# Optimization experiments

Measured on AMD Instinct MI355X. Metric: run time of the kernel, lower is better.

The kernel has to match this reference:

```python
import jax, jax.numpy as jnp
import numpy as np

DIM = 768
HEADS = 12
HIDDEN = 3072
EPS = 1e-5


def _layernorm(x, g, b):
    mu = jnp.mean(x, axis=-1, keepdims=True)
    var = jnp.var(x, axis=-1, keepdims=True)
    return (x - mu) * jax.lax.rsqrt(var + EPS) * g + b


def setup_inputs() -> dict:
    key = jax.random.key(0)
    ks = jax.random.split(key, 10)
    s_in = 1.0 / np.sqrt(DIM)
    s_hid = 1.0 / np.sqrt(HIDDEN)
    return {
        "x": jax.random.normal(ks[0], (8, 1024, DIM), dtype=jnp.float32),
        "ln1_g": jnp.ones((DIM,), jnp.float32),
        "ln1_b": jnp.zeros((DIM,), jnp.float32),
        "qkv_w": jax.random.uniform(ks[1], (DIM, 3 * DIM), jnp.float32, -s_in, s_in),
        "qkv_b": jnp.zeros((3 * DIM,), jnp.float32),
        "proj_w": jax.random.uniform(ks[2], (DIM, DIM), jnp.float32, -s_in, s_in),
        "proj_b": jnp.zeros((DIM,), jnp.float32),
        "ln2_g": jnp.ones((DIM,), jnp.float32),
        "ln2_b": jnp.zeros((DIM,), jnp.float32),
        "fc1_w": jax.random.uniform(ks[3], (DIM, HIDDEN), jnp.float32, -s_in, s_in),
        "fc1_b": jnp.zeros((HIDDEN,), jnp.float32),
        "fc2_w": jax.random.uniform(ks[4], (HIDDEN, DIM), jnp.float32, -s_hid, s_hid),
        "fc2_b": jnp.zeros((DIM,), jnp.float32),
    }


def reference(x, ln1_g, ln1_b, qkv_w, qkv_b, proj_w, proj_b,
              ln2_g, ln2_b, fc1_w, fc1_b, fc2_w, fc2_b):
    B, N, C = x.shape
    H = HEADS
    Dh = C // H
    scale = Dh ** -0.5

    # --- attention sublayer (pre-norm) ---
    h = _layernorm(x, ln1_g, ln1_b)
    qkv = h @ qkv_w + qkv_b  # [B,N,3C]
    qkv = qkv.reshape(B, N, 3, H, Dh)
    q = qkv[:, :, 0].transpose(0, 2, 1, 3)  # [B,H,N,Dh]
    k = qkv[:, :, 1].transpose(0, 2, 1, 3)
    v = qkv[:, :, 2].transpose(0, 2, 1, 3)
    attn = jax.nn.softmax(jnp.einsum('bhnd,bhmd->bhnm', q, k) * scale, axis=-1)
    o = jnp.einsum('bhnm,bhmd->bhnd', attn, v)  # [B,H,N,Dh]
    o = o.transpose(0, 2, 1, 3).reshape(B, N, C)
    x = x + (o @ proj_w + proj_b)

    # --- MLP sublayer (pre-norm) ---
    h = _layernorm(x, ln2_g, ln2_b)
    h = jax.nn.gelu(h @ fc1_w + fc1_b, approximate=False)
    x = x + (h @ fc2_w + fc2_b)
    return x
```

## Files before the change

kernel.cpp:

```cpp
#include <hip/hip_runtime.h>
#include <math.h>

#define DIM    768
#define HEADS  12
#define HIDDEN 3072
#define SEQ    1024
#define NTOK   8192
#define QKVLD  2304

typedef __bf16 bf16_t;
typedef __bf16 bf16x4 __attribute__((ext_vector_type(4)));
typedef __bf16 bf16x8 __attribute__((ext_vector_type(8)));
typedef float  f32x4  __attribute__((ext_vector_type(4)));

union ABFrag { bf16x4 h[2]; bf16x8 v; };

__device__ __forceinline__ void gload16(const void* g, void* l) {
  __builtin_amdgcn_global_load_lds(
      (const __attribute__((address_space(1))) void*)g,
      (__attribute__((address_space(3))) void*)l, 16, 0, 0);
}

__device__ __forceinline__ f32x4 mfma16(bf16x8 a, bf16x8 b, f32x4 c) {
  return __builtin_amdgcn_mfma_f32_16x16x32_bf16(a, b, c, 0, 0, 0);
}

__device__ __forceinline__ ABFrag load_frag(const bf16_t* rowp, int g) {
  ABFrag f;
  f.h[0] = *(const bf16x4*)(rowp + 4 * g);
  f.h[1] = *(const bf16x4*)(rowp + 4 * g + 16);
  return f;
}

__device__ __forceinline__ bf16x8 ldsfrag(const bf16_t* base, int row, int lc) {
  return *(const bf16x8*)(base + row * 64 + ((lc ^ (row & 7)) << 3));
}

__device__ __forceinline__ float gelu_f(float v) {
  float u = v * fmaf(v * v, 0.0356774081f, 0.7978845608f);
  u = fminf(u, 15.0f);
  float t = __builtin_amdgcn_exp2f(u * 2.8853900817779268f);
  return v * t * __builtin_amdgcn_rcpf(t + 1.0f);
}

__global__ __launch_bounds__(256) void ln_kernel(
    const float* __restrict__ x, const float* __restrict__ gw,
    const float* __restrict__ bw, bf16_t* __restrict__ out) {
  const int row = blockIdx.x * 4 + (threadIdx.x >> 6);
  const int lane = threadIdx.x & 63;
  const float* xr = x + (size_t)row * DIM;
  f32x4 v[3];
  float s = 0.f, s2 = 0.f;
  #pragma unroll
  for (int i = 0; i < 3; ++i) {
    v[i] = *(const f32x4*)(xr + lane * 4 + i * 256);
    #pragma unroll
    for (int j = 0; j < 4; ++j) { s += v[i][j]; s2 += v[i][j] * v[i][j]; }
  }
  #pragma unroll
  for (int o = 32; o > 0; o >>= 1) {
    s += __shfl_xor(s, o);
    s2 += __shfl_xor(s2, o);
  }
  const float mu  = s * (1.0f / DIM);
  const float var = s2 * (1.0f / DIM) - mu * mu;
  const float rs  = rsqrtf(var + 1e-5f);
  bf16_t* orow = out + (size_t)row * DIM;
  #pragma unroll
  for (int i = 0; i < 3; ++i) {
    const int c = lane * 4 + i * 256;
    f32x4 gv = *(const f32x4*)(gw + c);
    f32x4 bv = *(const f32x4*)(bw + c);
    bf16x4 o4;
    #pragma unroll
    for (int j = 0; j < 4; ++j)
      o4[j] = (bf16_t)((v[i][j] - mu) * rs * gv[j] + bv[j]);
    *(bf16x4*)(orow + c) = o4;
  }
}

__global__ __launch_bounds__(256) void wtrans_kernel(
    const float* __restrict__ W, bf16_t* __restrict__ Wt, int K, int N) {
  __shared__ float tile[32][33];
  const int tx = threadIdx.x, ty = threadIdx.y;
  const int n0 = blockIdx.x * 32, k0 = blockIdx.y * 32;
  #pragma unroll
  for (int i = 0; i < 4; ++i)
    tile[ty + i * 8][tx] = W[(size_t)(k0 + ty + i * 8) * N + n0 + tx];
  __syncthreads();
  #pragma unroll
  for (int i = 0; i < 4; ++i)
    Wt[(size_t)(n0 + ty + i * 8) * K + k0 + tx] = (bf16_t)tile[tx][ty + i * 8];
}

__global__ __launch_bounds__(256) void vtrans_kernel(
    const bf16_t* __restrict__ qkv, bf16_t* __restrict__ vt) {
  __shared__ bf16_t tile[64][65];
  const int bh = blockIdx.y, b = bh / HEADS, h = bh % HEADS;
  const int n0 = blockIdx.x * 64;
  const int t = threadIdx.x;
  const int c = t & 63, rr = t >> 6;
  const bf16_t* src = qkv + (size_t)(b * SEQ + n0) * QKVLD + 2 * DIM + h * 64;
  #pragma unroll
  for (int i = 0; i < 16; ++i)
    tile[c][rr + i * 4] = src[(size_t)(rr + i * 4) * QKVLD + c];
  __syncthreads();
  bf16_t* dst = vt + (size_t)bh * 64 * SEQ + n0;
  #pragma unroll
  for (int i = 0; i < 16; ++i)
    dst[(size_t)(rr + i * 4) * SEQ + c] = tile[rr + i * 4][c];
}

template <int MODE>
__global__ __launch_bounds__(256) void gemm_sb(
    const bf16_t* __restrict__ A, const bf16_t* __restrict__ Bt,
    int N, int K,
    const float* __restrict__ bias, const float* __restrict__ res,
    void* __restrict__ outv, int gx) {
  __shared__ bf16_t sA[128 * 64];
  __shared__ bf16_t sB[128 * 64];
  const int tid = threadIdx.x;
  const int lane = tid & 63;
  const int wid = tid >> 6;
  const int g = lane >> 4, r16 = lane & 15;

  const int nwg = gridDim.x;
  const int cpx = nwg >> 3;
  const int sw = (blockIdx.x & 7) * cpx + (blockIdx.x >> 3);
  const int bx = sw % gx, by = sw / gx;
  const int row0 = by * 128, col0 = bx * 128;
  const int wr = (wid >> 1) * 64, wc = (wid & 1) * 64;

  f32x4 acc[4][4];
  #pragma unroll
  for (int m = 0; m < 4; ++m)
    #pragma unroll
    for (int n = 0; n < 4; ++n) acc[m][n] = f32x4{0.f, 0.f, 0.f, 0.f};

  const int kSteps = K >> 6;
  for (int kt = 0; kt < kSteps; ++kt) {
    __syncthreads();
    #pragma unroll
    for (int rnd = 0; rnd < 4; ++rnd) {
      const int c = rnd * 256 + tid;
      const int row = c >> 3, scp = (c & 7) ^ (row & 7);
      gload16(A + (size_t)(row0 + row) * K + (size_t)kt * 64 + scp * 8, &sA[c * 8]);
    }
    #pragma unroll
    for (int rnd = 0; rnd < 4; ++rnd) {
      const int c = rnd * 256 + tid;
      const int row = c >> 3, scp = (c & 7) ^ (row & 7);
      gload16(Bt + (size_t)(col0 + row) * K + (size_t)kt * 64 + scp * 8, &sB[c * 8]);
    }
    __syncthreads();
    bf16x8 af[4][2], bfr[4][2];
    #pragma unroll
    for (int m = 0; m < 4; ++m)
      #pragma unroll
      for (int kk = 0; kk < 2; ++kk)
        af[m][kk] = ldsfrag(sA, wr + m * 16 + r16, kk * 4 + g);
    #pragma unroll
    for (int n = 0; n < 4; ++n)
      #pragma unroll
      for (int kk = 0; kk < 2; ++kk)
        bfr[n][kk] = ldsfrag(sB, wc + n * 16 + r16, kk * 4 + g);
    #pragma unroll
    for (int kk = 0; kk < 2; ++kk)
      #pragma unroll
      for (int m = 0; m < 4; ++m)
        #pragma unroll
        for (int n = 0; n < 4; ++n)
          acc[m][n] = mfma16(af[m][kk], bfr[n][kk], acc[m][n]);
  }

  #pragma unroll
  for (int m = 0; m < 4; ++m) {
    const int rowb = row0 + wr + m * 16 + 4 * g;
    #pragma unroll
    for (int n = 0; n < 4; ++n) {
      const int col = col0 + wc + n * 16 + r16;
      const float bv = bias[col];
      #pragma unroll
      for (int r = 0; r < 4; ++r) {
        const size_t idx = (size_t)(rowb + r) * N + col;
        float v = acc[m][n][r] + bv;
        if (MODE == 0) {
          ((bf16_t*)outv)[idx] = (bf16_t)v;
        } else if (MODE == 1) {
          ((float*)outv)[idx] = v + res[idx];
        } else {
          ((bf16_t*)outv)[idx] = (bf16_t)gelu_f(v);
        }
      }
    }
  }
}

template <int MODE>
__global__ __launch_bounds__(256) void gemm_db(
    const bf16_t* __restrict__ A, const bf16_t* __restrict__ Bt,
    int N, int K,
    const float* __restrict__ bias, const float* __restrict__ res,
    void* __restrict__ outv, int gx) {
  __shared__ bf16_t sA[2][128 * 64];
  __shared__ bf16_t sB[2][128 * 64];
  const int tid = threadIdx.x;
  const int lane = tid & 63;
  const int wid = tid >> 6;
  const int g = lane >> 4, r16 = lane & 15;

  const int nwg = gridDim.x;
  const int cpx = nwg >> 3;
  const int sw = (blockIdx.x & 7) * cpx + (blockIdx.x >> 3);
  const int bx = sw % gx, by = sw / gx;
  const int row0 = by * 128, col0 = bx * 128;
  const int wr = (wid >> 1) * 64, wc = (wid & 1) * 64;

  auto stage = [&](int p, int kt) {
    #pragma unroll
    for (int rnd = 0; rnd < 4; ++rnd) {
      const int c = rnd * 256 + tid;
      const int row = c >> 3, scp = (c & 7) ^ (row & 7);
      gload16(A + (size_t)(row0 + row) * K + (size_t)kt * 64 + scp * 8,
              &sA[p][c * 8]);
    }
    #pragma unroll
    for (int rnd = 0; rnd < 4; ++rnd) {
      const int c = rnd * 256 + tid;
      const int row = c >> 3, scp = (c & 7) ^ (row & 7);
      gload16(Bt + (size_t)(col0 + row) * K + (size_t)kt * 64 + scp * 8,
              &sB[p][c * 8]);
    }
  };

  f32x4 acc[4][4];
  #pragma unroll
  for (int m = 0; m < 4; ++m)
    #pragma unroll
    for (int n = 0; n < 4; ++n) acc[m][n] = f32x4{0.f, 0.f, 0.f, 0.f};

  const int kSteps = K >> 6;
  stage(0, 0);
  for (int kt = 0; kt < kSteps; ++kt) {
    const int cur = kt & 1;
    __syncthreads();
    if (kt + 1 < kSteps) stage(cur ^ 1, kt + 1);

    bf16x8 af[4][2], bfr[4][2];
    #pragma unroll
    for (int m = 0; m < 4; ++m)
      #pragma unroll
      for (int kk = 0; kk < 2; ++kk)
        af[m][kk] = ldsfrag(&sA[cur][0], wr + m * 16 + r16, kk * 4 + g);
    #pragma unroll
    for (int n = 0; n < 4; ++n)
      #pragma unroll
      for (int kk = 0; kk < 2; ++kk)
        bfr[n][kk] = ldsfrag(&sB[cur][0], wc + n * 16 + r16, kk * 4 + g);
    #pragma unroll
    for (int kk = 0; kk < 2; ++kk)
      #pragma unroll
      for (int m = 0; m < 4; ++m)
        #pragma unroll
        for (int n = 0; n < 4; ++n)
          acc[m][n] = mfma16(af[m][kk], bfr[n][kk], acc[m][n]);
  }

  #pragma unroll
  for (int m = 0; m < 4; ++m) {
    const int rowb = row0 + wr + m * 16 + 4 * g;
    #pragma unroll
    for (int n = 0; n < 4; ++n) {
      const int col = col0 + wc + n * 16 + r16;
      const float bv = bias[col];
      #pragma unroll
      for (int r = 0; r < 4; ++r) {
        const size_t idx = (size_t)(rowb + r) * N + col;
        float v = acc[m][n][r] + bv;
        if (MODE == 0) {
          ((bf16_t*)outv)[idx] = (bf16_t)v;
        } else if (MODE == 1) {
          ((float*)outv)[idx] = v + res[idx];
        } else {
          ((bf16_t*)outv)[idx] = (bf16_t)gelu_f(v);
        }
      }
    }
  }
}

__global__ __launch_bounds__(512) void attn_kernel(
    const bf16_t* __restrict__ qkv, const bf16_t* __restrict__ vt,
    bf16_t* __restrict__ o) {
  __shared__ bf16_t kbuf[2][64 * 64];
  __shared__ bf16_t vbuf[2][64 * 64];
  const int bh = blockIdx.x, b = bh / HEADS, h = bh % HEADS;
  const int q0 = blockIdx.y * 128;
  const int tid = threadIdx.x, lane = tid & 63, wid = tid >> 6;
  const int g = lane >> 4, r16 = lane & 15;

  const bf16_t* qptr = qkv + (size_t)b * SEQ * QKVLD + h * 64;
  const bf16_t* kptr = qptr + DIM;
  const bf16_t* vtp  = vt + (size_t)bh * 64 * SEQ;

  ABFrag aq[2];
  {
    const bf16_t* qr = qptr + (size_t)(q0 + wid * 16 + r16) * QKVLD;
    aq[0] = load_frag(qr, g);
    aq[1] = load_frag(qr + 32, g);
  }

  int off[4][2][2];
  #pragma unroll
  for (int i = 0; i < 4; ++i) {
    const int row = i * 16 + r16, s = row & 7, rp = row * 64;
    #pragma unroll
    for (int e2 = 0; e2 < 2; ++e2) {
      const int o0 = e2 * 32 + 4 * g, o1 = o0 + 16;
      off[i][e2][0] = rp + ((((o0 >> 3) ^ s) << 3) | (o0 & 7));
      off[i][e2][1] = rp + ((((o1 >> 3) ^ s) << 3) | (o1 & 7));
    }
  }

  float lacc = 0.f;
  f32x4 acco[4];
  #pragma unroll
  for (int n = 0; n < 4; ++n) acco[n] = f32x4{0.f, 0.f, 0.f, 0.f};

  const int srow = tid >> 3, sscp = (tid & 7) ^ (srow & 7);
  const bf16_t* kSrc = kptr + (size_t)srow * QKVLD + sscp * 8;
  const bf16_t* vSrc = vtp + (size_t)srow * SEQ + sscp * 8;
  auto stage = [&](int buf, int kv0) {
    gload16(kSrc + (size_t)kv0 * QKVLD, &kbuf[buf][tid * 8]);
    gload16(vSrc + kv0, &vbuf[buf][tid * 8]);
  };

  const float C2 = 0.125f * 1.4426950408889634f;

  stage(0, 0);
  for (int it = 0; it < SEQ / 64; ++it) {
    const int cur = it & 1;
    __syncthreads();
    if (it + 1 < SEQ / 64) stage(cur ^ 1, (it + 1) * 64);
    const bf16_t* kb = kbuf[cur];
    const bf16_t* vb = vbuf[cur];

    f32x4 st[4];
    __builtin_amdgcn_s_setprio(1);
    #pragma unroll
    for (int t = 0; t < 4; ++t) {
      st[t] = f32x4{0.f, 0.f, 0.f, 0.f};
      ABFrag ak0, ak1;
      ak0.h[0] = *(const bf16x4*)(kb + off[t][0][0]);
      ak0.h[1] = *(const bf16x4*)(kb + off[t][0][1]);
      st[t] = mfma16(ak0.v, aq[0].v, st[t]);
      ak1.h[0] = *(const bf16x4*)(kb + off[t][1][0]);
      ak1.h[1] = *(const bf16x4*)(kb + off[t][1][1]);
      st[t] = mfma16(ak1.v, aq[1].v, st[t]);
    }
    __builtin_amdgcn_s_setprio(0);

    float p[4][4];
    #pragma unroll
    for (int t = 0; t < 4; ++t)
      #pragma unroll
      for (int r = 0; r < 4; ++r) {
        float e = __builtin_amdgcn_exp2f(fmaf(st[t][r], C2, -16.0f));
        p[t][r] = e;
        lacc += e;
      }

    ABFrag pa0, pa1;
    #pragma unroll
    for (int r = 0; r < 4; ++r) {
      pa0.h[0][r] = (bf16_t)p[0][r];
      pa0.h[1][r] = (bf16_t)p[1][r];
      pa1.h[0][r] = (bf16_t)p[2][r];
      pa1.h[1][r] = (bf16_t)p[3][r];
    }

    __builtin_amdgcn_s_setprio(1);
    #pragma unroll
    for (int n = 0; n < 4; ++n) {
      ABFrag bv0, bv1;
      bv0.h[0] = *(const bf16x4*)(vb + off[n][0][0]);
      bv0.h[1] = *(const bf16x4*)(vb + off[n][0][1]);
      acco[n] = mfma16(pa0.v, bv0.v, acco[n]);
      bv1.h[0] = *(const bf16x4*)(vb + off[n][1][0]);
      bv1.h[1] = *(const bf16x4*)(vb + off[n][1][1]);
      acco[n] = mfma16(pa1.v, bv1.v, acco[n]);
    }
    __builtin_amdgcn_s_setprio(0);
  }

  float lt = lacc;
  lt += __shfl_xor(lt, 16);
  lt += __shfl_xor(lt, 32);
  float linv[4];
  #pragma unroll
  for (int r = 0; r < 4; ++r) linv[r] = 1.0f / __shfl(lt, 4 * g + r);
  bf16_t* op = o + (size_t)(b * SEQ + q0 + wid * 16 + 4 * g) * DIM + h * 64;
  #pragma unroll
  for (int n = 0; n < 4; ++n)
    #pragma unroll
    for (int r = 0; r < 4; ++r)
      op[(size_t)r * DIM + n * 16 + r16] = (bf16_t)(acco[n][r] * linv[r]);
}

extern "C" void kernel_launch(void* const* d_in, const int* in_sizes, int n_in,
                              void* d_out, int out_size, void* d_ws, size_t ws_size,
                              hipStream_t stream) {
  const float* x      = (const float*)d_in[0];
  const float* ln1_g  = (const float*)d_in[1];
  const float* ln1_b  = (const float*)d_in[2];
  const float* qkv_w  = (const float*)d_in[3];
  const float* qkv_b  = (const float*)d_in[4];
  const float* proj_w = (const float*)d_in[5];
  const float* proj_b = (const float*)d_in[6];
  const float* ln2_g  = (const float*)d_in[7];
  const float* ln2_b  = (const float*)d_in[8];
  const float* fc1_w  = (const float*)d_in[9];
  const float* fc1_b  = (const float*)d_in[10];
  const float* fc2_w  = (const float*)d_in[11];
  const float* fc2_b  = (const float*)d_in[12];
  float* out = (float*)d_out;

  char* ws = (char*)d_ws;
  size_t off = 0;
  auto alloc = [&](size_t bytes) -> void* {
    void* p = ws + off;
    off += (bytes + 255) & ~(size_t)255;
    return p;
  };
  bf16_t* wqkvT  = (bf16_t*)alloc((size_t)QKVLD * DIM * 2);
  bf16_t* wprojT = (bf16_t*)alloc((size_t)DIM * DIM * 2);
  bf16_t* wfc1T  = (bf16_t*)alloc((size_t)HIDDEN * DIM * 2);
  bf16_t* wfc2T  = (bf16_t*)alloc((size_t)DIM * HIDDEN * 2);
  bf16_t* buf1   = (bf16_t*)alloc((size_t)NTOK * DIM * 2);
  bf16_t* buf2   = (bf16_t*)alloc((size_t)NTOK * HIDDEN * 2);
  bf16_t* buf3   = (bf16_t*)alloc((size_t)NTOK * DIM * 2);
  float*  x1     = (float*)alloc((size_t)NTOK * DIM * 4);

  bf16_t* h1 = buf1;     bf16_t* obf = buf1;
  bf16_t* qkvbf = buf2;  bf16_t* h3 = buf2;
  bf16_t* vt = buf3;     bf16_t* h2 = buf3;
  (void)in_sizes; (void)n_in; (void)out_size; (void)ws_size;

  dim3 tb(32, 8);
  wtrans_kernel<<<dim3(QKVLD / 32, DIM / 32), tb, 0, stream>>>(qkv_w, wqkvT, DIM, QKVLD);
  wtrans_kernel<<<dim3(DIM / 32, DIM / 32), tb, 0, stream>>>(proj_w, wprojT, DIM, DIM);
  wtrans_kernel<<<dim3(HIDDEN / 32, DIM / 32), tb, 0, stream>>>(fc1_w, wfc1T, DIM, HIDDEN);
  wtrans_kernel<<<dim3(DIM / 32, HIDDEN / 32), tb, 0, stream>>>(fc2_w, wfc2T, HIDDEN, DIM);

  ln_kernel<<<NTOK / 4, 256, 0, stream>>>(x, ln1_g, ln1_b, h1);
  gemm_sb<0><<<(QKVLD / 128) * (NTOK / 128), 256, 0, stream>>>(
      h1, wqkvT, QKVLD, DIM, qkv_b, nullptr, qkvbf, QKVLD / 128);
  vtrans_kernel<<<dim3(SEQ / 64, 8 * HEADS), 256, 0, stream>>>(qkvbf, vt);
  attn_kernel<<<dim3(8 * HEADS, SEQ / 128), 512, 0, stream>>>(qkvbf, vt, obf);
  gemm_db<1><<<(DIM / 128) * (NTOK / 128), 256, 0, stream>>>(
      obf, wprojT, DIM, DIM, proj_b, x, x1, DIM / 128);
  ln_kernel<<<NTOK / 4, 256, 0, stream>>>(x1, ln2_g, ln2_b, h2);
  gemm_sb<2><<<(HIDDEN / 128) * (NTOK / 128), 256, 0, stream>>>(
      h2, wfc1T, HIDDEN, DIM, fc1_b, nullptr, h3, HIDDEN / 128);
  gemm_db<1><<<(DIM / 128) * (NTOK / 128), 256, 0, stream>>>(
      h3, wfc2T, DIM, HIDDEN, fc2_b, x1, out, DIM / 128);
}
```

Before: 256.2 us.

## Double-buffer QKV and FC1 GEMMs with 32-wide K tiles

```diff
diff --git a/kernel.cpp b/kernel.cpp
--- a/kernel.cpp
+++ b/kernel.cpp
@@ -34,6 +34,10 @@
 
 __device__ __forceinline__ bf16x8 ldsfrag(const bf16_t* base, int row, int lc) {
   return *(const bf16x8*)(base + row * 64 + ((lc ^ (row & 7)) << 3));
+}
+
+__device__ __forceinline__ bf16x8 ldsfrag32(const bf16_t* base, int row, int g) {
+  return *(const bf16x8*)(base + row * 32 + g * 8);
 }
 
 __device__ __forceinline__ float gelu_f(float v) {
@@ -112,13 +116,13 @@
 }
 
 template <int MODE>
-__global__ __launch_bounds__(256) void gemm_sb(
+__global__ __launch_bounds__(256) void gemm_db32(
     const bf16_t* __restrict__ A, const bf16_t* __restrict__ Bt,
     int N, int K,
     const float* __restrict__ bias, const float* __restrict__ res,
     void* __restrict__ outv, int gx) {
-  __shared__ bf16_t sA[128 * 64];
-  __shared__ bf16_t sB[128 * 64];
+  __shared__ bf16_t sA[2][128 * 32];
+  __shared__ bf16_t sB[2][128 * 32];
   const int tid = threadIdx.x;
   const int lane = tid & 63;
   const int wid = tid >> 6;
@@ -131,46 +135,44 @@
   const int row0 = by * 128, col0 = bx * 128;
   const int wr = (wid >> 1) * 64, wc = (wid & 1) * 64;
 
+  auto stage = [&](int p, int kt) {
+    #pragma unroll
+    for (int rnd = 0; rnd < 2; ++rnd) {
+      const int c = rnd * 256 + tid;
+      gload16(A + (size_t)(row0 + (c >> 2)) * K + (size_t)kt * 32 + (c & 3) * 8,
+              &sA[p][c * 8]);
+    }
+    #pragma unroll
+    for (int rnd = 0; rnd < 2; ++rnd) {
+      const int c = rnd * 256 + tid;
+      gload16(Bt + (size_t)(col0 + (c >> 2)) * K + (size_t)kt * 32 + (c & 3) * 8,
+              &sB[p][c * 8]);
+    }
+  };
+
   f32x4 acc[4][4];
   #pragma unroll
   for (int m = 0; m < 4; ++m)
     #pragma unroll
     for (int n = 0; n < 4; ++n) acc[m][n] = f32x4{0.f, 0.f, 0.f, 0.f};
 
-  const int kSteps = K >> 6;
+  const int kSteps = K >> 5;
+  stage(0, 0);
   for (int kt = 0; kt < kSteps; ++kt) {
+    const int cur = kt & 1;
     __syncthreads();
-    #pragma unroll
-    for (int rnd = 0; rnd < 4; ++rnd) {
-      const int c = rnd * 256 + tid;
-      const int row = c >> 3, scp = (c & 7) ^ (row & 7);
-      gload16(A + (size_t)(row0 + row) * K + (size_t)kt * 64 + scp * 8, &sA[c * 8]);
-    }
-    #pragma unroll
-    for (int rnd = 0; rnd < 4; ++rnd) {
-      const int c = rnd * 256 + tid;
-      const int row = c >> 3, scp = (c & 7) ^ (row & 7);
-      gload16(Bt + (size_t)(col0 + row) * K + (size_t)kt * 64 + scp * 8, &sB[c * 8]);
-    }
-    __syncthreads();
-    bf16x8 af[4][2], bfr[4][2];
+    if (kt + 1 < kSteps) stage(cur ^ 1, kt + 1);
+
+    bf16x8 af[4], bfr[4];
+    #pragma unroll
+    for (int m = 0; m < 4; ++m) af[m] = ldsfrag32(&sA[cur][0], wr + m * 16 + r16, g);
+    #pragma unroll
+    for (int n = 0; n < 4; ++n) bfr[n] = ldsfrag32(&sB[cur][0], wc + n * 16 + r16, g);
     #pragma unroll
     for (int m = 0; m < 4; ++m)
       #pragma unroll
-      for (int kk = 0; kk < 2; ++kk)
-        af[m][kk] = ldsfrag(sA, wr + m * 16 + r16, kk * 4 + g);
-    #pragma unroll
-    for (int n = 0; n < 4; ++n)
-      #pragma unroll
-      for (int kk = 0; kk < 2; ++kk)
-        bfr[n][kk] = ldsfrag(sB, wc + n * 16 + r16, kk * 4 + g);
-    #pragma unroll
-    for (int kk = 0; kk < 2; ++kk)
-      #pragma unroll
-      for (int m = 0; m < 4; ++m)
-        #pragma unroll
-        for (int n = 0; n < 4; ++n)
-          acc[m][n] = mfma16(af[m][kk], bfr[n][kk], acc[m][n]);
+      for (int n = 0; n < 4; ++n)
+        acc[m][n] = mfma16(af[m], bfr[n], acc[m][n]);
   }
 
   #pragma unroll
@@ -453,14 +455,14 @@
   wtrans_kernel<<<dim3(DIM / 32, HIDDEN / 32), tb, 0, stream>>>(fc2_w, wfc2T, HIDDEN, DIM);
 
   ln_kernel<<<NTOK / 4, 256, 0, stream>>>(x, ln1_g, ln1_b, h1);
-  gemm_sb<0><<<(QKVLD / 128) * (NTOK / 128), 256, 0, stream>>>(
+  gemm_db32<0><<<(QKVLD / 128) * (NTOK / 128), 256, 0, stream>>>(
       h1, wqkvT, QKVLD, DIM, qkv_b, nullptr, qkvbf, QKVLD / 128);
   vtrans_kernel<<<dim3(SEQ / 64, 8 * HEADS), 256, 0, stream>>>(qkvbf, vt);
   attn_kernel<<<dim3(8 * HEADS, SEQ / 128), 512, 0, stream>>>(qkvbf, vt, obf);
   gemm_db<1><<<(DIM / 128) * (NTOK / 128), 256, 0, stream>>>(
       obf, wprojT, DIM, DIM, proj_b, x, x1, DIM / 128);
   ln_kernel<<<NTOK / 4, 256, 0, stream>>>(x1, ln2_g, ln2_b, h2);
-  gemm_sb<2><<<(HIDDEN / 128) * (NTOK / 128), 256, 0, stream>>>(
+  gemm_db32<2><<<(HIDDEN / 128) * (NTOK / 128), 256, 0, stream>>>(
       h2, wfc1T, HIDDEN, DIM, fc1_b, nullptr, h3, HIDDEN / 128);
   gemm_db<1><<<(DIM / 128) * (NTOK / 128), 256, 0, stream>>>(
       h3, wfc2T, DIM, HIDDEN, fc2_b, x1, out, DIM / 128);
```

Measured after the change: 269.0 us. 5.0% more time.
